# Kernel optimization log

Measured on AMD Instinct MI355X. Metric: run time of the kernel, lower is better.

## Reference

```python
import jax, jax.numpy as jnp
import numpy as np

B, T, H, L = 32, 512, 1024, 2

def setup_inputs() -> dict:
    key = jax.random.key(0)
    k1, k2, k3 = jax.random.split(key, 3)
    scale = 1.0 / np.sqrt(H)
    x = jax.random.normal(k1, (B, T, H), dtype=jnp.float32)
    Wx = jax.random.normal(k2, (L, H, 4 * H), dtype=jnp.float32) * scale
    Wh = jax.random.normal(k3, (L, H, 4 * H), dtype=jnp.float32) * scale
    b = jnp.zeros((L, 4 * H), dtype=jnp.float32)
    return {"x": x, "Wx": Wx, "Wh": Wh, "b": b}


def _lstm_stack(x, Wx, Wh, b):
    # x: [B,T,H]; Wx,Wh: [L,H,4H] (gate order i,f,g,o); b: [L,4H]
    nl = Wx.shape[0]
    hdim = Wh.shape[1]
    bsz = x.shape[0]
    h0 = jnp.zeros((nl, bsz, hdim), dtype=x.dtype)
    c0 = jnp.zeros((nl, bsz, hdim), dtype=x.dtype)

    def step(carry, x_t):
        h, c = carry  # each [L,B,H]
        inp = x_t
        new_h, new_c = [], []
        for l in range(nl):
            z = inp @ Wx[l] + h[l] @ Wh[l] + b[l]  # [B,4H]
            zi, zf, zg, zo = jnp.split(z, 4, axis=-1)
            c_l = jax.nn.sigmoid(zf) * c[l] + jax.nn.sigmoid(zi) * jnp.tanh(zg)
            h_l = jax.nn.sigmoid(zo) * jnp.tanh(c_l)
            new_h.append(h_l)
            new_c.append(c_l)
            inp = h_l
        return (jnp.stack(new_h, 0), jnp.stack(new_c, 0)), inp

    (h_f, c_f), y_seq = jax.lax.scan(step, (h0, c0), jnp.swapaxes(x, 0, 1))
    y = jnp.swapaxes(y_seq, 0, 1)  # [B,T,H]
    return y, h_f, c_f


def reference(x, Wx, Wh, b):
    return _lstm_stack(x, Wx, Wh, b)
```

## Files before the change

### kernel.cpp

```cpp
#include <hip/hip_runtime.h>
#include <hip/hip_bf16.h>


typedef __attribute__((ext_vector_type(8))) short short8;
typedef __attribute__((ext_vector_type(4))) float f32x4;

__device__ __forceinline__ unsigned short f2bu(float f) {
    __hip_bfloat16 h = __float2bfloat16(f);
    return *(unsigned short*)&h;
}
__device__ __forceinline__ float b2f(unsigned short u) {
    __hip_bfloat16 h = *(__hip_bfloat16*)&u;
    return __bfloat162float(h);
}

__device__ __forceinline__ void gl_lds16(const unsigned short* gp, unsigned short* lp) {
    __builtin_amdgcn_global_load_lds(
        (__attribute__((address_space(1))) void*)gp,
        (__attribute__((address_space(3))) void*)lp, 16, 0, 17);
}

__device__ __forceinline__ void ast8(unsigned short* p, unsigned long long v) {
    __hip_atomic_store((unsigned long long*)p, v, __ATOMIC_RELAXED, __HIP_MEMORY_SCOPE_AGENT);
}
__device__ __forceinline__ unsigned alf(const unsigned* p) {
    return __hip_atomic_load(p, __ATOMIC_RELAXED, __HIP_MEMORY_SCOPE_AGENT);
}
__device__ __forceinline__ f32x4 mfma16(short8 a, short8 b, f32x4 c) {
    return __builtin_amdgcn_mfma_f32_16x16x32_bf16(a, b, c, 0, 0, 0);
}

__global__ __launch_bounds__(256) void pack_x(const float* __restrict__ x,
                                              unsigned short* __restrict__ xb) {
    int i = blockIdx.x * 256 + threadIdx.x;
    float4 v = ((const float4*)x)[i];
    ushort4 o;
    o.x = f2bu(v.x); o.y = f2bu(v.y); o.z = f2bu(v.z); o.w = f2bu(v.w);
    ((ushort4*)xb)[i] = o;
}

__global__ __launch_bounds__(256) void pack_w(const float* __restrict__ Wx,
                                              const float* __restrict__ Wh,
                                              unsigned short* __restrict__ Wxp,
                                              unsigned short* __restrict__ Whp0,
                                              unsigned short* __restrict__ Wcat) {
    __shared__ float tile[32][257];
    int mi = blockIdx.x >> 9;
    int rem = blockIdx.x & 511;
    int kb = rem >> 4;
    int cb = rem & 15;
    const float* src = (mi == 0) ? Wx : (mi == 1) ? (Wx + 4194304)
                     : (mi == 2) ? Wh : (Wh + 4194304);
    int tid = threadIdx.x;
    for (int pphase = 0; pphase < 8; ++pphase) {
        int row = pphase * 4 + (tid >> 6);
        int col4 = (tid & 63) * 4;
        float4 v = *(const float4*)(src + (size_t)(kb * 32 + row) * 4096 + cb * 256 + col4);
        tile[row][col4 + 0] = v.x; tile[row][col4 + 1] = v.y;
        tile[row][col4 + 2] = v.z; tile[row][col4 + 3] = v.w;
    }
    __syncthreads();
    int j = tid;
    int oc = cb * 256 + j;
    int gate = oc >> 10, hc = oc & 1023, w = hc >> 3, c = hc & 7;
    int p = w * 32 + gate * 8 + c;
    unsigned short* dst;
    if (mi == 0)      dst = Wxp  + (size_t)p * 1024 + kb * 32;
    else if (mi == 2) dst = Whp0 + (size_t)p * 1024 + kb * 32;
    else if (mi == 1) dst = Wcat + (size_t)p * 2048 + kb * 32;
    else              dst = Wcat + (size_t)p * 2048 + 1024 + kb * 32;
    for (int k = 0; k < 32; ++k) dst[k] = f2bu(tile[k][j]);
}

__global__ __launch_bounds__(256) void pack_misc(const float* __restrict__ b,
                                                 float* __restrict__ biasp,
                                                 unsigned* __restrict__ bars,
                                                 unsigned* __restrict__ hz) {
    int i = blockIdx.x * 256 + threadIdx.x;
    if (i < 4096) {
        int w = i >> 5, q = i & 31, gate = q >> 3, c = q & 7;
        biasp[i] = b[gate * 1024 + w * 8 + c];
    }
    if (i < 1024) bars[i] = 0u;
    hz[i] = 0u;
}

__global__ __launch_bounds__(256) void gemm_zx(const unsigned short* __restrict__ A,
                                               const unsigned short* __restrict__ Bt,
                                               const float* __restrict__ biasp,
                                               unsigned short* __restrict__ Zx) {
    __shared__ unsigned short Ash[128 * 72];
    __shared__ unsigned short Bsh[128 * 72];
    int tid = threadIdx.x;
    int bn = blockIdx.x & 31, bm = blockIdx.x >> 5;
    int L = tid & 63, wv = tid >> 6;
    int wm = (wv >> 1) * 64, wn = (wv & 1) * 64;
    f32x4 acc[4][4];
    for (int mi = 0; mi < 4; ++mi)
        for (int ni = 0; ni < 4; ++ni)
            acc[mi][ni] = (f32x4){0.f, 0.f, 0.f, 0.f};
    const int rs = tid >> 3;
    const int ch = tid & 7;
    for (int kt = 0; kt < 16; ++kt) {
        int k0 = kt * 64;
        __syncthreads();
#pragma unroll
        for (int it = 0; it < 4; ++it) {
            int r = it * 32 + rs;
            short8 av = *(const short8*)(A + (size_t)(bm * 128 + r) * 1024 + k0 + ch * 8);
            short8 bv = *(const short8*)(Bt + (size_t)(bn * 128 + r) * 1024 + k0 + ch * 8);
            *(short8*)(Ash + r * 72 + ch * 8) = av;
            *(short8*)(Bsh + r * 72 + ch * 8) = bv;
        }
        __syncthreads();
#pragma unroll
        for (int ks = 0; ks < 2; ++ks) {
            int ko = ks * 32 + (L >> 4) * 8;
            short8 af[4], bfv[4];
#pragma unroll
            for (int i = 0; i < 4; ++i)
                af[i] = *(const short8*)(Ash + (wm + i * 16 + (L & 15)) * 72 + ko);
#pragma unroll
            for (int i = 0; i < 4; ++i)
                bfv[i] = *(const short8*)(Bsh + (wn + i * 16 + (L & 15)) * 72 + ko);
#pragma unroll
            for (int mi = 0; mi < 4; ++mi)
#pragma unroll
                for (int ni = 0; ni < 4; ++ni)
                    acc[mi][ni] = mfma16(af[mi], bfv[ni], acc[mi][ni]);
        }
    }
#pragma unroll
    for (int mi = 0; mi < 4; ++mi) {
        int gr0 = bm * 128 + wm + mi * 16 + (L >> 4) * 4;
#pragma unroll
        for (int i = 0; i < 4; ++i) {
            int gr = gr0 + i;
            int bnat = gr >> 9, t = gr & 511;
#pragma unroll
            for (int ni = 0; ni < 4; ++ni) {
                int p = bn * 128 + wn + ni * 16 + (L & 15);
                float v = acc[mi][ni][i] + biasp[p];
                size_t addr = (((size_t)(p >> 5) * 512 + t) * 32 + bnat) * 32 + (p & 31);
                Zx[addr] = f2bu(v);
            }
        }
    }
}

__device__ __forceinline__ void stage_chunk(const unsigned short* __restrict__ ap,
                                            int koff,
                                            unsigned short* __restrict__ buf,
                                            int L) {
    int r = L >> 3;
    int b = (L & 7) * 16;
#pragma unroll
    for (int i = 0; i < 4; ++i) {
        int row = i * 8 + r;
        int e = (b ^ ((row & 7) << 4)) >> 1;
        gl_lds16(ap + (size_t)row * 1024 + koff + e, buf + i * 512);
    }
}

template<int LAY>
__device__ __forceinline__ void mfma_chunks(const unsigned short* __restrict__ ap,
                                            int kbase,
                                            unsigned short* __restrict__ b0,
                                            unsigned short* __restrict__ b1,
                                            unsigned short* __restrict__ b2,
                                            const short8 (&bfr)[2][16],
                                            int L, int quad, int m_r,
                                            f32x4 (&acc)[2][2]) {
    constexpr int NC = LAY ? 8 : 4;
    stage_chunk(ap, kbase, b0, L);
    stage_chunk(ap, kbase + 64, b1, L);
    stage_chunk(ap, kbase + 128, b2, L);
    const int S = (m_r & 7) << 4;
    const int e0 = ((quad * 16) ^ S) >> 1;
    const int e1 = ((64 + quad * 16) ^ S) >> 1;
#pragma unroll
    for (int c = 0; c < NC; ++c) {
        unsigned short* bc = (c % 3 == 0) ? b0 : (c % 3 == 1) ? b1 : b2;
        if (NC - 1 - c >= 2)      { asm volatile("s_waitcnt vmcnt(8)" ::: "memory"); }
        else if (NC - 1 - c == 1) { asm volatile("s_waitcnt vmcnt(4)" ::: "memory"); }
        else                      { asm volatile("s_waitcnt vmcnt(0)" ::: "memory"); }
        __builtin_amdgcn_sched_barrier(0);
        short8 a00 = *(const short8*)(bc + m_r * 64 + e0);
        short8 a10 = *(const short8*)(bc + (16 + m_r) * 64 + e0);
        short8 a01 = *(const short8*)(bc + m_r * 64 + e1);
        short8 a11 = *(const short8*)(bc + (16 + m_r) * 64 + e1);
        asm volatile("s_waitcnt lgkmcnt(0)" ::: "memory");
        __builtin_amdgcn_sched_barrier(0);
        if (c + 3 < NC) stage_chunk(ap, kbase + (c + 3) * 64, bc, L);
        acc[0][0] = mfma16(a00, bfr[0][2 * c], acc[0][0]);
        acc[0][1] = mfma16(a00, bfr[1][2 * c], acc[0][1]);
        acc[1][0] = mfma16(a10, bfr[0][2 * c], acc[1][0]);
        acc[1][1] = mfma16(a10, bfr[1][2 * c], acc[1][1]);
        acc[0][0] = mfma16(a01, bfr[0][2 * c + 1], acc[0][0]);
        acc[0][1] = mfma16(a01, bfr[1][2 * c + 1], acc[0][1]);
        acc[1][0] = mfma16(a11, bfr[0][2 * c + 1], acc[1][0]);
        acc[1][1] = mfma16(a11, bfr[1][2 * c + 1], acc[1][1]);
    }
}

__global__ __launch_bounds__(256, 1) void lstm_fused(
        const unsigned short* __restrict__ Whp0,
        const unsigned short* __restrict__ Wcat,
        const unsigned short* __restrict__ Zx,
        const float* __restrict__ bias,
        unsigned short* __restrict__ h0buf,
        unsigned short* __restrict__ h1buf,
        unsigned* __restrict__ flags,
        float* __restrict__ out) {
    __shared__ unsigned short ash[4][3][2048];
    __shared__ unsigned long long zx8[256];
    __shared__ unsigned long long hl8[32];
    unsigned short* zxloc = (unsigned short*)zx8;
    unsigned short* hloc  = (unsigned short*)hl8;

    int tid = threadIdx.x, wgid = blockIdx.x;
    int lay = wgid >> 7, w = wgid & 127;
    int L = tid & 63, wv = tid >> 6;
    int m_r = L & 15, quad = L >> 4;
    int nk = lay ? 16 : 8;
    int K  = lay ? 2048 : 1024;
    unsigned short* b0 = &ash[wv][0][0];
    unsigned short* b1 = &ash[wv][1][0];
    unsigned short* b2 = &ash[wv][2][0];
    float* zsw = (float*)&ash[wv][0][0];

    short8 bfr[2][16];
    {
        const unsigned short* wb = lay ? (Wcat + (size_t)w * 32 * 2048)
                                       : (Whp0 + (size_t)w * 32 * 1024);
        for (int nt = 0; nt < 2; ++nt)
            for (int ks = 0; ks < nk; ++ks) {
                int n = nt * 16 + m_r;
                int k = wv * (K / 4) + ks * 32 + quad * 8;
                bfr[nt][ks] = *(const short8*)(wb + (size_t)n * K + k);
            }
    }
    int gb = tid >> 3, gc = tid & 7;
    float bi0 = 0.f, bf0 = 0.f, bg0 = 0.f, bo0 = 0.f;
    if (lay) {
        bi0 = bias[4096 + 0 * 1024 + w * 8 + gc];
        bf0 = bias[4096 + 1 * 1024 + w * 8 + gc];
        bg0 = bias[4096 + 2 * 1024 + w * 8 + gc];
        bo0 = bias[4096 + 3 * 1024 + w * 8 + gc];
    }
    float creg = 0.f;

    for (int s = 0; s < 513; ++s) {
        int t = lay ? s - 1 : s;
        bool active = lay ? (s >= 1) : (s < 512);

        if (active) {
            const unsigned short* h0p = h0buf + ((s + 1) & 1) * 32768;
            const unsigned short* h1p = h1buf + ((s + 1) & 1) * 32768;
            const unsigned short* ap = (lay && wv >= 2) ? h1p : h0p;
            int kbase = lay ? ((wv >= 2) ? wv * 512 - 1024 : wv * 512) : wv * 256;
            if (!lay) {
                const unsigned long long* zb =
                    (const unsigned long long*)(Zx + ((size_t)w * 512 + t) * 1024);
                zx8[tid] = zb[tid];
            }
            f32x4 acc[2][2];
            for (int a = 0; a < 2; ++a)
                for (int bq = 0; bq < 2; ++bq)
                    acc[a][bq] = (f32x4){0.f, 0.f, 0.f, 0.f};
            if (lay) mfma_chunks<1>(ap, kbase, b0, b1, b2, bfr, L, quad, m_r, acc);
            else     mfma_chunks<0>(ap, kbase, b0, b1, b2, bfr, L, quad, m_r, acc);
#pragma unroll
            for (int mt = 0; mt < 2; ++mt)
#pragma unroll
                for (int nt = 0; nt < 2; ++nt)
#pragma unroll
                    for (int i = 0; i < 4; ++i)
                        zsw[(mt * 16 + quad * 4 + i) * 32 + nt * 16 + m_r] = acc[mt][nt][i];
        }
        __syncthreads();

        float hval = 0.f, cnv = 0.f;
        if (active) {
            float zi = bi0, zf = bf0, zg = bg0, zo = bo0;
#pragma unroll
            for (int v = 0; v < 4; ++v) {
                const float* zv = (const float*)&ash[v][0][0];
                zi += zv[gb * 32 + gc];      zf += zv[gb * 32 + 8 + gc];
                zg += zv[gb * 32 + 16 + gc]; zo += zv[gb * 32 + 24 + gc];
            }
            if (!lay) {
                zi += b2f(zxloc[gb * 32 + gc]);      zf += b2f(zxloc[gb * 32 + 8 + gc]);
                zg += b2f(zxloc[gb * 32 + 16 + gc]); zo += b2f(zxloc[gb * 32 + 24 + gc]);
            }
            float si = 1.f / (1.f + __expf(-zi));
            float sf = 1.f / (1.f + __expf(-zf));
            float so = 1.f / (1.f + __expf(-zo));
            cnv = sf * creg + si * tanhf(zg);
            creg = cnv;
            hval = so * tanhf(cnv);
            hloc[gb * 8 + gc] = f2bu(hval);
        }
        __syncthreads();

        if (active && tid < 64) {
            int br = tid >> 1, half = tid & 1;
            unsigned long long v = *(unsigned long long*)(hloc + br * 8 + half * 4);
            unsigned short* dst = (lay ? h1buf : h0buf) + (s & 1) * 32768
                                  + br * 1024 + w * 8 + half * 4;
            ast8(dst, v);
        }
        __syncthreads();
        unsigned tgt = (unsigned)s + 1u;
        if (tid == 0)
            __hip_atomic_store(flags + wgid, tgt, __ATOMIC_RELAXED, __HIP_MEMORY_SCOPE_AGENT);
        if (wgid == 0 && tid < 64) {
            for (;;) {
                unsigned f0 = alf(flags + tid);
                unsigned f1 = alf(flags + 64 + tid);
                unsigned f2 = alf(flags + 128 + tid);
                unsigned f3 = alf(flags + 192 + tid);
                if (__all((f0 >= tgt) && (f1 >= tgt) && (f2 >= tgt) && (f3 >= tgt))) break;
                __builtin_amdgcn_s_sleep(2);
            }
            if (tid < 8)
                __hip_atomic_store(flags + 320 + tid * 32, tgt, __ATOMIC_RELAXED, __HIP_MEMORY_SCOPE_AGENT);
        }
        if (active) {
            if (lay) {
                out[((size_t)gb * 512 + t) * 1024 + w * 8 + gc] = hval;
                if (t == 511) {
                    out[16777216 + 32768 + gb * 1024 + w * 8 + gc] = hval;
                    out[16777216 + 65536 + 32768 + gb * 1024 + w * 8 + gc] = cnv;
                }
            } else if (t == 511) {
                out[16777216 + gb * 1024 + w * 8 + gc] = hval;
                out[16777216 + 65536 + gb * 1024 + w * 8 + gc] = cnv;
            }
        }
        if (tid == 0) {
            unsigned* g = flags + 320 + (wgid & 7) * 32;
            while (alf(g) < tgt)
                __builtin_amdgcn_s_sleep(2);
        }
        __syncthreads();
    }
}

extern "C" void kernel_launch(void* const* d_in, const int* in_sizes, int n_in,
                              void* d_out, int out_size, void* d_ws, size_t ws_size,
                              hipStream_t stream) {
    const float* x  = (const float*)d_in[0];
    const float* Wx = (const float*)d_in[1];
    const float* Wh = (const float*)d_in[2];
    const float* bb = (const float*)d_in[3];

    char* ws = (char*)d_ws;
    unsigned short* Wxp  = (unsigned short*)ws;
    unsigned short* Whp0 = (unsigned short*)(ws + (8ull  << 20));
    unsigned short* Wcat = (unsigned short*)(ws + (16ull << 20));
    unsigned short* xb   = (unsigned short*)(ws + (32ull << 20));
    unsigned short* Zx   = (unsigned short*)(ws + (64ull << 20));
    char* misc           = ws + (192ull << 20);
    float* biasp         = (float*)misc;
    unsigned* bars       = (unsigned*)(misc + (64 << 10));
    unsigned short* h0b  = (unsigned short*)(misc + (128 << 10));
    unsigned short* h1b  = (unsigned short*)(misc + (256 << 10));
    unsigned* hz         = (unsigned*)(misc + (128 << 10));

    float* out = (float*)d_out;

    pack_x<<<16384, 256, 0, stream>>>(x, xb);
    pack_w<<<2048, 256, 0, stream>>>(Wx, Wh, Wxp, Whp0, Wcat);
    pack_misc<<<256, 256, 0, stream>>>(bb, biasp, bars, hz);

    gemm_zx<<<4096, 256, 0, stream>>>(xb, Wxp, biasp, Zx);
    lstm_fused<<<256, 256, 0, stream>>>(Whp0, Wcat, Zx, bb, h0b, h1b, bars, out);
}
```

Measured before the change: 3.969 ms.

## Split global step barrier into per-layer generation flags with 4-slot h buffers

Replaces the single all-workgroup barrier per time step with separate generation counters: layer 0 waits only on layer-0 completion (plus a lagged check on layer 1 for buffer reuse), and layer 1 splits its matmul into an h0 part and an h1 part, each gated by its own flag. The h buffers grow from double to quadruple buffering so producers can run ahead without overwriting data still being read. This aims to shorten the per-step critical path by letting layer-1 work overlap with layer-0 progress. It costs more coordinator polling and extra buffer memory, and the lagged write-after-read conditions are delicate to get right.

New measurement: 3.885 ms. 2.1% less time.

```diff
diff --git a/kernel.cpp b/kernel.cpp
--- a/kernel.cpp
+++ b/kernel.cpp
@@ -22,6 +22,9 @@
 
 __device__ __forceinline__ void ast8(unsigned short* p, unsigned long long v) {
     __hip_atomic_store((unsigned long long*)p, v, __ATOMIC_RELAXED, __HIP_MEMORY_SCOPE_AGENT);
+}
+__device__ __forceinline__ void astf(unsigned* p, unsigned v) {
+    __hip_atomic_store(p, v, __ATOMIC_RELAXED, __HIP_MEMORY_SCOPE_AGENT);
 }
 __device__ __forceinline__ unsigned alf(const unsigned* p) {
     return __hip_atomic_load(p, __ATOMIC_RELAXED, __HIP_MEMORY_SCOPE_AGENT);
@@ -81,8 +84,9 @@
         int w = i >> 5, q = i & 31, gate = q >> 3, c = q & 7;
         biasp[i] = b[gate * 1024 + w * 8 + c];
     }
-    if (i < 1024) bars[i] = 0u;
+    if (i < 2048) bars[i] = 0u;
     hz[i] = 0u;
+    hz[i + 65536] = 0u;
 }
 
 __global__ __launch_bounds__(256) void gemm_zx(const unsigned short* __restrict__ A,
@@ -162,16 +166,14 @@
     }
 }
 
-template<int LAY>
-__device__ __forceinline__ void mfma_chunks(const unsigned short* __restrict__ ap,
-                                            int kbase,
-                                            unsigned short* __restrict__ b0,
-                                            unsigned short* __restrict__ b1,
-                                            unsigned short* __restrict__ b2,
-                                            const short8 (&bfr)[2][16],
-                                            int L, int quad, int m_r,
-                                            f32x4 (&acc)[2][2]) {
-    constexpr int NC = LAY ? 8 : 4;
+__device__ __forceinline__ void mfma_chunks4(const unsigned short* __restrict__ ap,
+                                             int kbase, int bofs,
+                                             unsigned short* __restrict__ b0,
+                                             unsigned short* __restrict__ b1,
+                                             unsigned short* __restrict__ b2,
+                                             const short8 (&bfr)[2][16],
+                                             int L, int quad, int m_r,
+                                             f32x4 (&acc)[2][2]) {
     stage_chunk(ap, kbase, b0, L);
     stage_chunk(ap, kbase + 64, b1, L);
     stage_chunk(ap, kbase + 128, b2, L);
@@ -179,11 +181,11 @@
     const int e0 = ((quad * 16) ^ S) >> 1;
     const int e1 = ((64 + quad * 16) ^ S) >> 1;
 #pragma unroll
-    for (int c = 0; c < NC; ++c) {
-        unsigned short* bc = (c % 3 == 0) ? b0 : (c % 3 == 1) ? b1 : b2;
-        if (NC - 1 - c >= 2)      { asm volatile("s_waitcnt vmcnt(8)" ::: "memory"); }
-        else if (NC - 1 - c == 1) { asm volatile("s_waitcnt vmcnt(4)" ::: "memory"); }
-        else                      { asm volatile("s_waitcnt vmcnt(0)" ::: "memory"); }
+    for (int c = 0; c < 4; ++c) {
+        unsigned short* bc = (c == 0 || c == 3) ? b0 : (c == 1) ? b1 : b2;
+        if (c <= 1)      { asm volatile("s_waitcnt vmcnt(8)" ::: "memory"); }
+        else if (c == 2) { asm volatile("s_waitcnt vmcnt(4)" ::: "memory"); }
+        else             { asm volatile("s_waitcnt vmcnt(0)" ::: "memory"); }
         __builtin_amdgcn_sched_barrier(0);
         short8 a00 = *(const short8*)(bc + m_r * 64 + e0);
         short8 a10 = *(const short8*)(bc + (16 + m_r) * 64 + e0);
@@ -191,15 +193,15 @@
         short8 a11 = *(const short8*)(bc + (16 + m_r) * 64 + e1);
         asm volatile("s_waitcnt lgkmcnt(0)" ::: "memory");
         __builtin_amdgcn_sched_barrier(0);
-        if (c + 3 < NC) stage_chunk(ap, kbase + (c + 3) * 64, bc, L);
-        acc[0][0] = mfma16(a00, bfr[0][2 * c], acc[0][0]);
-        acc[0][1] = mfma16(a00, bfr[1][2 * c], acc[0][1]);
-        acc[1][0] = mfma16(a10, bfr[0][2 * c], acc[1][0]);
-        acc[1][1] = mfma16(a10, bfr[1][2 * c], acc[1][1]);
-        acc[0][0] = mfma16(a01, bfr[0][2 * c + 1], acc[0][0]);
-        acc[0][1] = mfma16(a01, bfr[1][2 * c + 1], acc[0][1]);
-        acc[1][0] = mfma16(a11, bfr[0][2 * c + 1], acc[1][0]);
-        acc[1][1] = mfma16(a11, bfr[1][2 * c + 1], acc[1][1]);
+        if (c == 0) stage_chunk(ap, kbase + 192, bc, L);
+        acc[0][0] = mfma16(a00, bfr[0][bofs + 2 * c], acc[0][0]);
+        acc[0][1] = mfma16(a00, bfr[1][bofs + 2 * c], acc[0][1]);
+        acc[1][0] = mfma16(a10, bfr[0][bofs + 2 * c], acc[1][0]);
+        acc[1][1] = mfma16(a10, bfr[1][bofs + 2 * c], acc[1][1]);
+        acc[0][0] = mfma16(a01, bfr[0][bofs + 2 * c + 1], acc[0][0]);
+        acc[0][1] = mfma16(a01, bfr[1][bofs + 2 * c + 1], acc[0][1]);
+        acc[1][0] = mfma16(a11, bfr[0][bofs + 2 * c + 1], acc[1][0]);
+        acc[1][1] = mfma16(a11, bfr[1][bofs + 2 * c + 1], acc[1][1]);
     }
 }
 
@@ -236,7 +238,10 @@
         for (int nt = 0; nt < 2; ++nt)
             for (int ks = 0; ks < nk; ++ks) {
                 int n = nt * 16 + m_r;
-                int k = wv * (K / 4) + ks * 32 + quad * 8;
+                int k;
+                if (!lay)        k = wv * 256 + ks * 32 + quad * 8;
+                else if (ks < 8) k = wv * 256 + ks * 32 + quad * 8;
+                else             k = 1024 + wv * 256 + (ks - 8) * 32 + quad * 8;
                 bfr[nt][ks] = *(const short8*)(wb + (size_t)n * K + k);
             }
     }
@@ -249,27 +254,49 @@
         bo0 = bias[4096 + 3 * 1024 + w * 8 + gc];
     }
     float creg = 0.f;
+    const unsigned* genA = flags + 320 + (wgid & 7) * 32;
+    const unsigned* genB = flags + 576 + (wgid & 7) * 32;
+    const unsigned* genC = flags + 832 + (wgid & 7) * 32;
 
     for (int s = 0; s < 513; ++s) {
         int t = lay ? s - 1 : s;
         bool active = lay ? (s >= 1) : (s < 512);
-
+        int rdslot = ((s + 3) & 3) * 32768;
+        int wrslot = (s & 3) * 32768;
+
+        f32x4 acc[2][2];
+        for (int a = 0; a < 2; ++a)
+            for (int bq = 0; bq < 2; ++bq)
+                acc[a][bq] = (f32x4){0.f, 0.f, 0.f, 0.f};
+
+        if (!lay) {
+            if (tid == 0)
+                while (alf(genA) < (unsigned)s) __builtin_amdgcn_s_sleep(2);
+            __syncthreads();
+            if (active) {
+                if (true) {
+                    const unsigned long long* zb =
+                        (const unsigned long long*)(Zx + ((size_t)w * 512 + t) * 1024);
+                    zx8[tid] = zb[tid];
+                }
+                mfma_chunks4(h0buf + rdslot, wv * 256, 0, b0, b1, b2,
+                             bfr, L, quad, m_r, acc);
+            }
+        } else {
+            if (tid == 0)
+                while (alf(genB) < (unsigned)s) __builtin_amdgcn_s_sleep(2);
+            __syncthreads();
+            if (active)
+                mfma_chunks4(h0buf + rdslot, wv * 256, 0, b0, b1, b2,
+                             bfr, L, quad, m_r, acc);
+            if (tid == 0)
+                while (alf(genC) < (unsigned)s) __builtin_amdgcn_s_sleep(2);
+            __syncthreads();
+            if (active)
+                mfma_chunks4(h1buf + rdslot, wv * 256, 8, b0, b1, b2,
+                             bfr, L, quad, m_r, acc);
+        }
         if (active) {
-            const unsigned short* h0p = h0buf + ((s + 1) & 1) * 32768;
-            const unsigned short* h1p = h1buf + ((s + 1) & 1) * 32768;
-            const unsigned short* ap = (lay && wv >= 2) ? h1p : h0p;
-            int kbase = lay ? ((wv >= 2) ? wv * 512 - 1024 : wv * 512) : wv * 256;
-            if (!lay) {
-                const unsigned long long* zb =
-                    (const unsigned long long*)(Zx + ((size_t)w * 512 + t) * 1024);
-                zx8[tid] = zb[tid];
-            }
-            f32x4 acc[2][2];
-            for (int a = 0; a < 2; ++a)
-                for (int bq = 0; bq < 2; ++bq)
-                    acc[a][bq] = (f32x4){0.f, 0.f, 0.f, 0.f};
-            if (lay) mfma_chunks<1>(ap, kbase, b0, b1, b2, bfr, L, quad, m_r, acc);
-            else     mfma_chunks<0>(ap, kbase, b0, b1, b2, bfr, L, quad, m_r, acc);
 #pragma unroll
             for (int mt = 0; mt < 2; ++mt)
 #pragma unroll
@@ -306,25 +333,39 @@
         if (active && tid < 64) {
             int br = tid >> 1, half = tid & 1;
             unsigned long long v = *(unsigned long long*)(hloc + br * 8 + half * 4);
-            unsigned short* dst = (lay ? h1buf : h0buf) + (s & 1) * 32768
+            unsigned short* dst = (lay ? h1buf : h0buf) + wrslot
                                   + br * 1024 + w * 8 + half * 4;
             ast8(dst, v);
         }
         __syncthreads();
         unsigned tgt = (unsigned)s + 1u;
-        if (tid == 0)
-            __hip_atomic_store(flags + wgid, tgt, __ATOMIC_RELAXED, __HIP_MEMORY_SCOPE_AGENT);
+        if (tid == 0) astf(flags + wgid, tgt);
+
         if (wgid == 0 && tid < 64) {
+            unsigned warL1 = (tgt > 2u) ? tgt - 2u : 0u;
             for (;;) {
                 unsigned f0 = alf(flags + tid);
                 unsigned f1 = alf(flags + 64 + tid);
-                unsigned f2 = alf(flags + 128 + tid);
-                unsigned f3 = alf(flags + 192 + tid);
-                if (__all((f0 >= tgt) && (f1 >= tgt) && (f2 >= tgt) && (f3 >= tgt))) break;
+                unsigned g0 = alf(flags + 128 + tid);
+                unsigned g1 = alf(flags + 192 + tid);
+                if (__all((f0 >= tgt) && (f1 >= tgt) && (g0 >= warL1) && (g1 >= warL1)))
+                    break;
                 __builtin_amdgcn_s_sleep(2);
             }
-            if (tid < 8)
-                __hip_atomic_store(flags + 320 + tid * 32, tgt, __ATOMIC_RELAXED, __HIP_MEMORY_SCOPE_AGENT);
+            if (tid < 8)       astf(flags + 320 + tid * 32, tgt);
+            else if (tid < 16) astf(flags + 576 + (tid - 8) * 32, tgt);
+        }
+        if (wgid == 128 && tid < 64) {
+            for (;;) {
+                unsigned f0 = alf(flags + tid);
+                unsigned f1 = alf(flags + 64 + tid);
+                unsigned g0 = alf(flags + 128 + tid);
+                unsigned g1 = alf(flags + 192 + tid);
+                if (__all((f0 >= tgt) && (f1 >= tgt) && (g0 >= tgt) && (g1 >= tgt)))
+                    break;
+                __builtin_amdgcn_s_sleep(2);
+            }
+            if (tid < 8) astf(flags + 832 + tid * 32, tgt);
         }
         if (active) {
             if (lay) {
@@ -338,12 +379,6 @@
                 out[16777216 + 65536 + gb * 1024 + w * 8 + gc] = cnv;
             }
         }
-        if (tid == 0) {
-            unsigned* g = flags + 320 + (wgid & 7) * 32;
-            while (alf(g) < tgt)
-                __builtin_amdgcn_s_sleep(2);
-        }
-        __syncthreads();
     }
 }
 
@@ -365,7 +400,7 @@
     float* biasp         = (float*)misc;
     unsigned* bars       = (unsigned*)(misc + (64 << 10));
     unsigned short* h0b  = (unsigned short*)(misc + (128 << 10));
-    unsigned short* h1b  = (unsigned short*)(misc + (256 << 10));
+    unsigned short* h1b  = (unsigned short*)(misc + (384 << 10));
     unsigned* hz         = (unsigned*)(misc + (128 << 10));
 
     float* out = (float*)d_out;
```
